# Optimization experiments

Measured on AMD Instinct MI355X. Metric: run time of the kernel, lower is better.

The kernel has to match this reference:

```python
import jax, jax.numpy as jnp
import numpy as np

B, S, D = 2, 2048, 512
WIN = 64  # local causal window (includes current token)
EPS = 1e-5


def setup_inputs() -> dict:
    key = jax.random.key(0)
    ks = jax.random.split(key, 8)
    sc = 0.02
    return {
        "x":  jax.random.normal(ks[0], (B, S, D), jnp.float32),
        "Wq": jax.random.normal(ks[1], (D, D), jnp.float32) * sc,
        "bq": jnp.zeros((D,), jnp.float32),
        "Wk": jax.random.normal(ks[2], (D, D), jnp.float32) * sc,
        "bk": jnp.zeros((D,), jnp.float32),
        "Wv": jax.random.normal(ks[3], (D, D), jnp.float32) * sc,
        "bv": jnp.zeros((D,), jnp.float32),
        "Wo": jax.random.normal(ks[4], (D, D), jnp.float32) * sc,
        "bo": jnp.zeros((D,), jnp.float32),
        "Wr": jax.random.normal(ks[5], (D, D), jnp.float32) * sc,
        "br": jnp.zeros((D,), jnp.float32),
        "gamma": jnp.ones((D,), jnp.float32),
        "beta":  jnp.zeros((D,), jnp.float32),
    }


def _layernorm(h, gamma, beta):
    mu = jnp.mean(h, axis=-1, keepdims=True)
    var = jnp.mean(jnp.square(h - mu), axis=-1, keepdims=True)
    return (h - mu) * jax.lax.rsqrt(var + EPS) * gamma + beta


def _local_attention(x, Wq, bq, Wk, bk, Wv, bv, Wo, bo):
    q = x @ Wq + bq
    k = x @ Wk + bk
    v = x @ Wv + bv
    kp = jnp.pad(k, ((0, 0), (WIN - 1, 0), (0, 0)))
    vp = jnp.pad(v, ((0, 0), (WIN - 1, 0), (0, 0)))
    idx = jnp.arange(S)[:, None] + jnp.arange(WIN)[None, :]
    kw = kp[:, idx, :]
    vw = vp[:, idx, :]
    scores = jnp.einsum('bsd,bswd->bsw', q, kw) / np.float32(np.sqrt(D))
    valid = (idx >= (WIN - 1 - jnp.zeros((), jnp.int32)))  # padded slots invalid
    valid = idx >= (WIN - 1) - jnp.arange(S)[:, None] * 0
    valid = (idx - (WIN - 1)) >= 0  # key position in original seq >= 0
    scores = jnp.where(valid[None, :, :], scores, jnp.float32(-1e9))
    attn = jax.nn.softmax(scores, axis=-1)
    out = jnp.einsum('bsw,bswd->bsd', attn, vw)
    return out @ Wo + bo


def reference(x, Wq, bq, Wk, bk, Wv, bv, Wo, bo, Wr, br, gamma, beta):
    read = _local_attention(x, Wq, bq, Wk, bk, Wv, bv, Wo, bo)
    sence = x @ Wr + br
    read = _layernorm(read, gamma, beta)
    sence = _layernorm(sence, gamma, beta)
    return jax.nn.gelu(read + sence, approximate=False)
```

## Files before the change

### kernel.cpp

```cpp
#include <hip/hip_runtime.h>
#include <hip/hip_bf16.h>
#include <math.h>

#define BB 2
#define SS 2048
#define DD 512
#define MTOT 4096
#define WINW 64

typedef __attribute__((ext_vector_type(8))) short sv8;
typedef __attribute__((ext_vector_type(4))) float f32x4;

static const size_t OFF_XB   = 0;
static const size_t OFF_WT   = 4194304;
static const size_t OFF_BIAS = 6815744;
static const size_t OFF_Y    = 6823936;
static const size_t OFF_ATT  = 23601152;
static const size_t OFF_READ = 27795456;

static __device__ __forceinline__ float bf2f(short s) {
    unsigned u = ((unsigned)(unsigned short)s) << 16;
    return __builtin_bit_cast(float, u);
}
static __device__ __forceinline__ short f2bf(float f) {
    unsigned u = __builtin_bit_cast(unsigned, f);
    unsigned r = 0x7fffu + ((u >> 16) & 1u);
    u += r;
    return (short)(u >> 16);
}

__global__ __launch_bounds__(256) void cast_x(const float* __restrict__ x,
                                              short* __restrict__ xb, int n4) {
    int i = blockIdx.x * 256 + threadIdx.x;
    if (i < n4) {
        float4 v = ((const float4*)x)[i];
        short4 o;
        o.x = f2bf(v.x); o.y = f2bf(v.y); o.z = f2bf(v.z); o.w = f2bf(v.w);
        ((short4*)xb)[i] = o;
    }
}

__global__ __launch_bounds__(256) void cast_w(const float* __restrict__ Wq,
                                              const float* __restrict__ Wk,
                                              const float* __restrict__ Wv,
                                              const float* __restrict__ Wr,
                                              const float* __restrict__ Wo,
                                              short* __restrict__ wt) {
    __shared__ float tile[32][33];
    int z = blockIdx.z;
    const float* W = (z == 0) ? Wq : (z == 1) ? Wk : (z == 2) ? Wv : (z == 3) ? Wr : Wo;
    int k0 = blockIdx.y * 32, n0 = blockIdx.x * 32;
    int tx = threadIdx.x & 31, ty = threadIdx.x >> 5;
    for (int r = ty; r < 32; r += 8)
        tile[r][tx] = W[(size_t)(k0 + r) * 512 + n0 + tx];
    __syncthreads();
    short* o = wt + (size_t)z * 512 * 512;
    for (int r = ty; r < 32; r += 8)
        o[(size_t)(n0 + r) * 512 + k0 + tx] = f2bf(tile[tx][r]);
}

__global__ __launch_bounds__(256) void prep_bias(const float* __restrict__ bq,
                                                 const float* __restrict__ bk,
                                                 const float* __restrict__ bv,
                                                 const float* __restrict__ br,
                                                 float* __restrict__ ball) {
    int i = blockIdx.x * 256 + threadIdx.x;
    int sel = i >> 9;
    const float* src = (sel == 0) ? bq : (sel == 1) ? bk : (sel == 2) ? bv : br;
    ball[i] = src[i & 511];
}

template <int OUT_F32>
__global__ __launch_bounds__(256) void gemm_bt(const short* __restrict__ A,
                                               const short* __restrict__ Bt,
                                               const float* __restrict__ bias,
                                               void* __restrict__ Cout, int ldc) {
    const int K = 512;
    const int LDL = 72;
    __shared__ __align__(16) short lA[128 * LDL];
    __shared__ __align__(16) short lB[128 * LDL];
    int tid = threadIdx.x;
    int mbase = blockIdx.y * 128;
    int nbase = blockIdx.x * 128;
    int lane = tid & 63, wave = tid >> 6;
    int wm = wave >> 1, wn = wave & 1;

    f32x4 acc[4][4] = {};

    for (int k0 = 0; k0 < K; k0 += 64) {
#pragma unroll
        for (int t = 0; t < 4; ++t) {
            int c = tid + t * 256;
            int row = c >> 3, slot = c & 7;
            sv8 va = *(const sv8*)(A + (size_t)(mbase + row) * K + k0 + slot * 8);
            *(sv8*)&lA[row * LDL + slot * 8] = va;
            sv8 vb = *(const sv8*)(Bt + (size_t)(nbase + row) * K + k0 + slot * 8);
            *(sv8*)&lB[row * LDL + slot * 8] = vb;
        }
        __syncthreads();
#pragma unroll
        for (int kk = 0; kk < 2; ++kk) {
            int koff = kk * 32 + (lane >> 4) * 8;
            sv8 af[4], bfr[4];
#pragma unroll
            for (int m = 0; m < 4; ++m)
                af[m] = *(const sv8*)&lA[(wm * 64 + m * 16 + (lane & 15)) * LDL + koff];
#pragma unroll
            for (int n = 0; n < 4; ++n)
                bfr[n] = *(const sv8*)&lB[(wn * 64 + n * 16 + (lane & 15)) * LDL + koff];
#pragma unroll
            for (int m = 0; m < 4; ++m)
#pragma unroll
                for (int n = 0; n < 4; ++n)
                    acc[m][n] = __builtin_amdgcn_mfma_f32_16x16x32_bf16(
                        af[m], bfr[n], acc[m][n], 0, 0, 0);
        }
        __syncthreads();
    }

    int r0 = (lane >> 4) * 4, c0 = lane & 15;
#pragma unroll
    for (int m = 0; m < 4; ++m) {
#pragma unroll
        for (int n = 0; n < 4; ++n) {
            int col = nbase + wn * 64 + n * 16 + c0;
            float bv = bias[col];
#pragma unroll
            for (int j = 0; j < 4; ++j) {
                int row = mbase + wm * 64 + m * 16 + r0 + j;
                float v = acc[m][n][j] + bv;
                if (OUT_F32)
                    ((float*)Cout)[(size_t)row * ldc + col] = v;
                else
                    ((short*)Cout)[(size_t)row * ldc + col] = f2bf(v);
            }
        }
    }
}

__global__ __launch_bounds__(256) void attn_kernel(const short* __restrict__ Y,
                                                   short* __restrict__ att) {
    int wave = threadIdx.x >> 6, lane = threadIdx.x & 63;
    int s = blockIdx.x * 4 + wave;
    int b = s >> 11, t = s & 2047;
    const short* q = Y + (size_t)s * 2048;
    const short* Kbase = Y + ((size_t)(b << 11)) * 2048 + 512;
    const short* Vbase = Y + ((size_t)(b << 11)) * 2048 + 1024;

    int jlane = t - 63 + lane;
    float score = -1e30f;
    if (jlane >= 0) {
        const short* krow = Kbase + (size_t)jlane * 2048;
        float acc = 0.f;
        for (int c = 0; c < 64; ++c) {
            sv8 qv = *(const sv8*)(q + c * 8);
            sv8 kv = *(const sv8*)(krow + c * 8);
#pragma unroll
            for (int e = 0; e < 8; ++e) acc += bf2f(qv[e]) * bf2f(kv[e]);
        }
        score = acc * 0.04419417382415922f;
    }
    float m = score;
#pragma unroll
    for (int off = 32; off; off >>= 1) m = fmaxf(m, __shfl_xor(m, off));
    float p = (jlane >= 0) ? __expf(score - m) : 0.f;
    float sum = p;
#pragma unroll
    for (int off = 32; off; off >>= 1) sum += __shfl_xor(sum, off);
    p /= sum;

    float o[8] = {0.f, 0.f, 0.f, 0.f, 0.f, 0.f, 0.f, 0.f};
    int w0 = (t >= 63) ? 0 : (63 - t);
    for (int w = w0; w < 64; ++w) {
        float pw = __shfl(p, w);
        const short* vrow = Vbase + (size_t)(t - 63 + w) * 2048;
        sv8 vv = *(const sv8*)(vrow + lane * 8);
#pragma unroll
        for (int e = 0; e < 8; ++e) o[e] += pw * bf2f(vv[e]);
    }
    sv8 ov;
#pragma unroll
    for (int e = 0; e < 8; ++e) ov[e] = f2bf(o[e]);
    *(sv8*)(att + (size_t)s * 512 + lane * 8) = ov;
}

__global__ __launch_bounds__(256) void ln_gelu(const float* __restrict__ readb,
                                               const short* __restrict__ Y,
                                               const float* __restrict__ gamma,
                                               const float* __restrict__ beta,
                                               float* __restrict__ out) {
    int s = blockIdx.x;
    int tid = threadIdx.x;
    const float* r = readb + (size_t)s * 512;
    const short* sn = Y + (size_t)s * 2048 + 1536;
    float r0 = r[tid], r1 = r[tid + 256];
    float s0 = bf2f(sn[tid]), s1 = bf2f(sn[tid + 256]);

    float v0 = r0 + r1, v1 = r0 * r0 + r1 * r1;
    float v2 = s0 + s1, v3 = s0 * s0 + s1 * s1;
#pragma unroll
    for (int off = 32; off; off >>= 1) {
        v0 += __shfl_xor(v0, off);
        v1 += __shfl_xor(v1, off);
        v2 += __shfl_xor(v2, off);
        v3 += __shfl_xor(v3, off);
    }
    __shared__ float red[4][4];
    int wave = tid >> 6, lane = tid & 63;
    if (lane == 0) {
        red[wave][0] = v0; red[wave][1] = v1; red[wave][2] = v2; red[wave][3] = v3;
    }
    __syncthreads();
    float t0 = red[0][0] + red[1][0] + red[2][0] + red[3][0];
    float t1 = red[0][1] + red[1][1] + red[2][1] + red[3][1];
    float t2 = red[0][2] + red[1][2] + red[2][2] + red[3][2];
    float t3 = red[0][3] + red[1][3] + red[2][3] + red[3][3];

    float mu_r = t0 * (1.f / 512.f);
    float var_r = t1 * (1.f / 512.f) - mu_r * mu_r;
    float is_r = rsqrtf(var_r + 1e-5f);
    float mu_s = t2 * (1.f / 512.f);
    float var_s = t3 * (1.f / 512.f) - mu_s * mu_s;
    float is_s = rsqrtf(var_s + 1e-5f);

    float g0 = gamma[tid], be0 = beta[tid];
    float g1 = gamma[tid + 256], be1 = beta[tid + 256];
    float x0 = (r0 - mu_r) * is_r * g0 + be0 + (s0 - mu_s) * is_s * g0 + be0;
    float x1 = (r1 - mu_r) * is_r * g1 + be1 + (s1 - mu_s) * is_s * g1 + be1;
    float y0 = 0.5f * x0 * (1.f + erff(x0 * 0.70710678118654752f));
    float y1 = 0.5f * x1 * (1.f + erff(x1 * 0.70710678118654752f));
    out[(size_t)s * 512 + tid] = y0;
    out[(size_t)s * 512 + tid + 256] = y1;
}

extern "C" void kernel_launch(void* const* d_in, const int* in_sizes, int n_in,
                              void* d_out, int out_size, void* d_ws, size_t ws_size,
                              hipStream_t stream) {
    const float* x  = (const float*)d_in[0];
    const float* Wq = (const float*)d_in[1];
    const float* bq = (const float*)d_in[2];
    const float* Wk = (const float*)d_in[3];
    const float* bk = (const float*)d_in[4];
    const float* Wv = (const float*)d_in[5];
    const float* bv = (const float*)d_in[6];
    const float* Wo = (const float*)d_in[7];
    const float* bo = (const float*)d_in[8];
    const float* Wr = (const float*)d_in[9];
    const float* br = (const float*)d_in[10];
    const float* gamma = (const float*)d_in[11];
    const float* beta  = (const float*)d_in[12];

    char* ws = (char*)d_ws;
    short* xb   = (short*)(ws + OFF_XB);
    short* wt   = (short*)(ws + OFF_WT);
    float* ball = (float*)(ws + OFF_BIAS);
    short* Y    = (short*)(ws + OFF_Y);
    short* att  = (short*)(ws + OFF_ATT);
    float* readb = (float*)(ws + OFF_READ);

    cast_x<<<2048, 256, 0, stream>>>(x, xb, MTOT * DD / 4);
    cast_w<<<dim3(16, 16, 5), 256, 0, stream>>>(Wq, Wk, Wv, Wr, Wo, wt);
    prep_bias<<<8, 256, 0, stream>>>(bq, bk, bv, br, ball);

    gemm_bt<0><<<dim3(16, 32), 256, 0, stream>>>(xb, wt, ball, Y, 2048);

    attn_kernel<<<1024, 256, 0, stream>>>(Y, att);

    gemm_bt<1><<<dim3(4, 32), 256, 0, stream>>>(att, wt + (size_t)4 * 512 * 512, bo,
                                                readb, 512);

    ln_gelu<<<4096, 256, 0, stream>>>(readb, Y, gamma, beta, (float*)d_out);
}
```

Baseline: 185.0 us.

## Recast sliding-window attention as MFMA tile GEMMs with transposed V

Replaces the scalar per-query attention kernel with two tiled MFMA kernels. The first computes a 64x128 score tile per 64-query block, applies the window mask and softmax, and writes bf16 probabilities. The second multiplies those probabilities by a transposed V that the QKV GEMM epilogue now writes directly. The output projection also stores bf16 instead of fp32 for the layernorm input, and the workspace is reused by placing att over the spent xb buffer. Risks: the scores kernel launches only 64 blocks, the PV kernel reads V slightly before the buffer for the first tile (those terms get zero weight), and bf16 storage of the read path costs precision.

New measurement: 149.5 us. 1.24x faster.

```diff
diff --git a/kernel.cpp b/kernel.cpp
--- a/kernel.cpp
+++ b/kernel.cpp
@@ -15,8 +15,10 @@
 static const size_t OFF_WT   = 4194304;
 static const size_t OFF_BIAS = 6815744;
 static const size_t OFF_Y    = 6823936;
-static const size_t OFF_ATT  = 23601152;
-static const size_t OFF_READ = 27795456;
+static const size_t OFF_VT   = 23601152;
+static const size_t OFF_PP   = 27795456;
+static const size_t OFF_ATT  = 0;
+static const size_t OFF_READ = 28844032;
 
 static __device__ __forceinline__ float bf2f(short s) {
     unsigned u = ((unsigned)(unsigned short)s) << 16;
@@ -70,11 +72,11 @@
     ball[i] = src[i & 511];
 }
 
-template <int OUT_F32>
 __global__ __launch_bounds__(256) void gemm_bt(const short* __restrict__ A,
                                                const short* __restrict__ Bt,
                                                const float* __restrict__ bias,
-                                               void* __restrict__ Cout, int ldc) {
+                                               short* __restrict__ Cout, int ldc,
+                                               short* __restrict__ vt) {
     const int K = 512;
     const int LDL = 72;
     __shared__ __align__(16) short lA[128 * LDL];
@@ -119,81 +121,180 @@
     }
 
     int r0 = (lane >> 4) * 4, c0 = lane & 15;
+    bool tovt = (vt != nullptr) && (nbase >= 1024) && (nbase < 1536);
 #pragma unroll
     for (int m = 0; m < 4; ++m) {
 #pragma unroll
         for (int n = 0; n < 4; ++n) {
             int col = nbase + wn * 64 + n * 16 + c0;
             float bv = bias[col];
+            if (tovt) {
+                int d = col - 1024;
+                int row0 = mbase + wm * 64 + m * 16 + r0;
+                int bb = row0 >> 11, t = row0 & 2047;
+                short4 o;
+                o.x = f2bf(acc[m][n][0] + bv);
+                o.y = f2bf(acc[m][n][1] + bv);
+                o.z = f2bf(acc[m][n][2] + bv);
+                o.w = f2bf(acc[m][n][3] + bv);
+                *(short4*)(vt + (size_t)(bb * 512 + d) * 2048 + t) = o;
+            } else {
+#pragma unroll
+                for (int j = 0; j < 4; ++j) {
+                    int row = mbase + wm * 64 + m * 16 + r0 + j;
+                    Cout[(size_t)row * ldc + col] = f2bf(acc[m][n][j] + bv);
+                }
+            }
+        }
+    }
+}
+
+__global__ __launch_bounds__(256) void attn_scores(const short* __restrict__ Y,
+                                                   short* __restrict__ Pp) {
+    __shared__ float sS[64][132];
+    int tile = blockIdx.x;
+    int b = tile >> 5;
+    int t0 = (tile & 31) * 64;
+    int s0 = tile * 64;
+    int tid = threadIdx.x, lane = tid & 63, wave = tid >> 6;
+    int wm = wave >> 1, wn = wave & 1;
+
+    f32x4 acc[2][4] = {};
+    const short* Q = Y;
+    const short* Kb = Y + 512;
+
+    int arow[2], brow[4];
+#pragma unroll
+    for (int m = 0; m < 2; ++m) arow[m] = s0 + wm * 32 + m * 16 + (lane & 15);
+#pragma unroll
+    for (int n = 0; n < 4; ++n) {
+        int kr = t0 - 64 + wn * 64 + n * 16 + (lane & 15);
+        if (kr < 0) kr = 0;
+        brow[n] = (b << 11) + kr;
+    }
+#pragma unroll
+    for (int step = 0; step < 16; ++step) {
+        int koff = step * 32 + (lane >> 4) * 8;
+        sv8 af[2], bfr[4];
+#pragma unroll
+        for (int m = 0; m < 2; ++m)
+            af[m] = *(const sv8*)(Q + (size_t)arow[m] * 2048 + koff);
+#pragma unroll
+        for (int n = 0; n < 4; ++n)
+            bfr[n] = *(const sv8*)(Kb + (size_t)brow[n] * 2048 + koff);
+#pragma unroll
+        for (int m = 0; m < 2; ++m)
+#pragma unroll
+            for (int n = 0; n < 4; ++n)
+                acc[m][n] = __builtin_amdgcn_mfma_f32_16x16x32_bf16(
+                    af[m], bfr[n], acc[m][n], 0, 0, 0);
+    }
+    int r0 = (lane >> 4) * 4, c0 = lane & 15;
+#pragma unroll
+    for (int m = 0; m < 2; ++m)
+#pragma unroll
+        for (int n = 0; n < 4; ++n) {
+            int jc = wn * 64 + n * 16 + c0;
+#pragma unroll
+            for (int j = 0; j < 4; ++j)
+                sS[wm * 32 + m * 16 + r0 + j][jc] =
+                    acc[m][n][j] * 0.04419417382415922f;
+        }
+    __syncthreads();
+
+    int q = tid >> 2, j0 = (tid & 3) * 32;
+    float v[32];
+    float mx = -1e30f;
+    int jlo = q + 1;
+    int jmin0 = 64 - t0;
+    if (jmin0 > jlo) jlo = jmin0;
+    int jhi = q + 64;
+#pragma unroll
+    for (int jj = 0; jj < 32; ++jj) {
+        int j = j0 + jj;
+        bool ok = (j >= jlo) && (j <= jhi);
+        float s = ok ? sS[q][j] : -1e30f;
+        v[jj] = s;
+        mx = fmaxf(mx, s);
+    }
+    mx = fmaxf(mx, __shfl_xor(mx, 1));
+    mx = fmaxf(mx, __shfl_xor(mx, 2));
+    float sum = 0.f;
+#pragma unroll
+    for (int jj = 0; jj < 32; ++jj) {
+        float e = (v[jj] > -1e29f) ? __expf(v[jj] - mx) : 0.f;
+        v[jj] = e;
+        sum += e;
+    }
+    sum += __shfl_xor(sum, 1);
+    sum += __shfl_xor(sum, 2);
+    float inv = 1.f / sum;
+    short* dst = Pp + (size_t)tile * 8192 + q * 128 + j0;
+#pragma unroll
+    for (int k = 0; k < 4; ++k) {
+        sv8 o;
+#pragma unroll
+        for (int e = 0; e < 8; ++e) o[e] = f2bf(v[k * 8 + e] * inv);
+        *(sv8*)(dst + k * 8) = o;
+    }
+}
+
+__global__ __launch_bounds__(256) void attn_pv(const short* __restrict__ Pp,
+                                               const short* __restrict__ Vt,
+                                               short* __restrict__ att) {
+    int tile = blockIdx.y, dchunk = blockIdx.x;
+    int b = tile >> 5;
+    int t0 = (tile & 31) * 64;
+    int s0 = tile * 64;
+    int tid = threadIdx.x, lane = tid & 63, wave = tid >> 6;
+    int wm = wave >> 1, wn = wave & 1;
+
+    f32x4 acc[2][4] = {};
+    const short* Pbase = Pp + (size_t)tile * 8192;
+#pragma unroll
+    for (int ks = 0; ks < 4; ++ks) {
+        int koff = ks * 32 + (lane >> 4) * 8;
+        sv8 af[2], bfr[4];
+#pragma unroll
+        for (int m = 0; m < 2; ++m)
+            af[m] = *(const sv8*)(Pbase + (wm * 32 + m * 16 + (lane & 15)) * 128 + koff);
+#pragma unroll
+        for (int n = 0; n < 4; ++n) {
+            int d = dchunk * 128 + wn * 64 + n * 16 + (lane & 15);
+            long off = (long)(b * 512 + d) * 2048 + (t0 - 64 + koff);
+            bfr[n] = *(const sv8*)(Vt + off);
+        }
+#pragma unroll
+        for (int m = 0; m < 2; ++m)
+#pragma unroll
+            for (int n = 0; n < 4; ++n)
+                acc[m][n] = __builtin_amdgcn_mfma_f32_16x16x32_bf16(
+                    af[m], bfr[n], acc[m][n], 0, 0, 0);
+    }
+    int r0 = (lane >> 4) * 4, c0 = lane & 15;
+#pragma unroll
+    for (int m = 0; m < 2; ++m)
+#pragma unroll
+        for (int n = 0; n < 4; ++n) {
+            int col = dchunk * 128 + wn * 64 + n * 16 + c0;
 #pragma unroll
             for (int j = 0; j < 4; ++j) {
-                int row = mbase + wm * 64 + m * 16 + r0 + j;
-                float v = acc[m][n][j] + bv;
-                if (OUT_F32)
-                    ((float*)Cout)[(size_t)row * ldc + col] = v;
-                else
-                    ((short*)Cout)[(size_t)row * ldc + col] = f2bf(v);
+                int row = s0 + wm * 32 + m * 16 + r0 + j;
+                att[(size_t)row * 512 + col] = f2bf(acc[m][n][j]);
             }
         }
-    }
-}
-
-__global__ __launch_bounds__(256) void attn_kernel(const short* __restrict__ Y,
-                                                   short* __restrict__ att) {
-    int wave = threadIdx.x >> 6, lane = threadIdx.x & 63;
-    int s = blockIdx.x * 4 + wave;
-    int b = s >> 11, t = s & 2047;
-    const short* q = Y + (size_t)s * 2048;
-    const short* Kbase = Y + ((size_t)(b << 11)) * 2048 + 512;
-    const short* Vbase = Y + ((size_t)(b << 11)) * 2048 + 1024;
-
-    int jlane = t - 63 + lane;
-    float score = -1e30f;
-    if (jlane >= 0) {
-        const short* krow = Kbase + (size_t)jlane * 2048;
-        float acc = 0.f;
-        for (int c = 0; c < 64; ++c) {
-            sv8 qv = *(const sv8*)(q + c * 8);
-            sv8 kv = *(const sv8*)(krow + c * 8);
-#pragma unroll
-            for (int e = 0; e < 8; ++e) acc += bf2f(qv[e]) * bf2f(kv[e]);
-        }
-        score = acc * 0.04419417382415922f;
-    }
-    float m = score;
-#pragma unroll
-    for (int off = 32; off; off >>= 1) m = fmaxf(m, __shfl_xor(m, off));
-    float p = (jlane >= 0) ? __expf(score - m) : 0.f;
-    float sum = p;
-#pragma unroll
-    for (int off = 32; off; off >>= 1) sum += __shfl_xor(sum, off);
-    p /= sum;
-
-    float o[8] = {0.f, 0.f, 0.f, 0.f, 0.f, 0.f, 0.f, 0.f};
-    int w0 = (t >= 63) ? 0 : (63 - t);
-    for (int w = w0; w < 64; ++w) {
-        float pw = __shfl(p, w);
-        const short* vrow = Vbase + (size_t)(t - 63 + w) * 2048;
-        sv8 vv = *(const sv8*)(vrow + lane * 8);
-#pragma unroll
-        for (int e = 0; e < 8; ++e) o[e] += pw * bf2f(vv[e]);
-    }
-    sv8 ov;
-#pragma unroll
-    for (int e = 0; e < 8; ++e) ov[e] = f2bf(o[e]);
-    *(sv8*)(att + (size_t)s * 512 + lane * 8) = ov;
-}
-
-__global__ __launch_bounds__(256) void ln_gelu(const float* __restrict__ readb,
+}
+
+__global__ __launch_bounds__(256) void ln_gelu(const short* __restrict__ readb,
                                                const short* __restrict__ Y,
                                                const float* __restrict__ gamma,
                                                const float* __restrict__ beta,
                                                float* __restrict__ out) {
     int s = blockIdx.x;
     int tid = threadIdx.x;
-    const float* r = readb + (size_t)s * 512;
+    const short* r = readb + (size_t)s * 512;
     const short* sn = Y + (size_t)s * 2048 + 1536;
-    float r0 = r[tid], r1 = r[tid + 256];
+    float r0 = bf2f(r[tid]), r1 = bf2f(r[tid + 256]);
     float s0 = bf2f(sn[tid]), s1 = bf2f(sn[tid + 256]);
 
     float v0 = r0 + r1, v1 = r0 * r0 + r1 * r1;
@@ -251,23 +352,26 @@
     const float* beta  = (const float*)d_in[12];
 
     char* ws = (char*)d_ws;
-    short* xb   = (short*)(ws + OFF_XB);
-    short* wt   = (short*)(ws + OFF_WT);
-    float* ball = (float*)(ws + OFF_BIAS);
-    short* Y    = (short*)(ws + OFF_Y);
-    short* att  = (short*)(ws + OFF_ATT);
-    float* readb = (float*)(ws + OFF_READ);
+    short* xb    = (short*)(ws + OFF_XB);
+    short* wt    = (short*)(ws + OFF_WT);
+    float* ball  = (float*)(ws + OFF_BIAS);
+    short* Y     = (short*)(ws + OFF_Y);
+    short* vtb   = (short*)(ws + OFF_VT);
+    short* Pp    = (short*)(ws + OFF_PP);
+    short* att   = (short*)(ws + OFF_ATT);
+    short* readb = (short*)(ws + OFF_READ);
 
     cast_x<<<2048, 256, 0, stream>>>(x, xb, MTOT * DD / 4);
     cast_w<<<dim3(16, 16, 5), 256, 0, stream>>>(Wq, Wk, Wv, Wr, Wo, wt);
     prep_bias<<<8, 256, 0, stream>>>(bq, bk, bv, br, ball);
 
-    gemm_bt<0><<<dim3(16, 32), 256, 0, stream>>>(xb, wt, ball, Y, 2048);
-
-    attn_kernel<<<1024, 256, 0, stream>>>(Y, att);
-
-    gemm_bt<1><<<dim3(4, 32), 256, 0, stream>>>(att, wt + (size_t)4 * 512 * 512, bo,
-                                                readb, 512);
+    gemm_bt<<<dim3(16, 32), 256, 0, stream>>>(xb, wt, ball, Y, 2048, vtb);
+
+    attn_scores<<<64, 256, 0, stream>>>(Y, Pp);
+    attn_pv<<<dim3(4, 64), 256, 0, stream>>>(Pp, vtb, att);
+
+    gemm_bt<<<dim3(4, 32), 256, 0, stream>>>(att, wt + (size_t)4 * 512 * 512, bo,
+                                             readb, 512, nullptr);
 
     ln_gelu<<<4096, 256, 0, stream>>>(readb, Y, gamma, beta, (float*)d_out);
 }
```
